# Kernel optimization log

Hardware: AMD Instinct MI355X
Metric: run time of the kernel (lower is better)

The kernel has to match this reference:

```python
import jax, jax.numpy as jnp
import numpy as np

BS, L, D, H, BLOCKS = 2, 8192, 1024, 16, 16
BC = L // BLOCKS          # block_ctx = 512
HD = D // H               # head dim = 64
SCALE2 = 1.0 / float(np.sqrt(HD))  # (scale*scale) with scale = HD**-0.25


def setup_inputs() -> dict:
    key = jax.random.key(0)
    k0, k1, k2 = jax.random.split(key, 3)
    return {
        "x": jax.random.normal(k0, (BS, L, D), jnp.float32),
        "w_attn": jax.random.normal(k1, (D, 3 * D), jnp.float32) * 0.02,
        "b_attn": jnp.zeros((3 * D,), jnp.float32),
        "w_proj": jax.random.normal(k2, (D, D), jnp.float32) * 0.02,
        "b_proj": jnp.zeros((D,), jnp.float32),
    }


def _block_attn(q, k, v):
    # q, k, v: [BS, L, D]; block-local causal attention (attn_func=1, eval path)
    nb = BS * BLOCKS
    def heads(x):
        # [BS, L, D] -> [nb, BC, D] -> [nb, H, BC, HD]
        return x.reshape(nb, BC, H, HD).transpose(0, 2, 1, 3)
    qh, kh, vh = heads(q), heads(k), heads(v)
    w = jnp.einsum('bhqd,bhkd->bhqk', qh, kh) * SCALE2          # [nb, H, BC, BC]
    w = w.astype(jnp.float32)
    mask = jnp.tril(jnp.ones((BC, BC), jnp.float32))
    w = w * mask + (-1e9) * (1.0 - mask)
    w = jax.nn.softmax(w, axis=-1)
    a = jnp.einsum('bhqk,bhkd->bhqd', w, vh)                    # [nb, H, BC, HD]
    return a.transpose(0, 2, 1, 3).reshape(BS, L, D)


def reference(x, w_attn, b_attn, w_proj, b_proj):
    qkv = x @ w_attn + b_attn                                   # Conv1D c_attn
    q, k, v = jnp.split(qkv, 3, axis=-1)
    a = _block_attn(q, k, v)
    return a @ w_proj + b_proj                                  # Conv1D c_proj
```

## Files before the change

### kernel.cpp

```cpp
#include <hip/hip_runtime.h>
#include <stdint.h>


typedef __bf16 bf16x8 __attribute__((ext_vector_type(8)));
typedef short short8 __attribute__((ext_vector_type(8)));
typedef float f32x4 __attribute__((ext_vector_type(4)));
typedef unsigned short ushort4v __attribute__((ext_vector_type(4)));
typedef unsigned short ushort8v __attribute__((ext_vector_type(8)));

#define GLOAD_LDS16(g, l)                                                      \
  __builtin_amdgcn_global_load_lds(                                            \
      (const __attribute__((address_space(1))) void*)(g),                      \
      (__attribute__((address_space(3))) void*)(l), 16, 0, 0)

static __device__ __forceinline__ f32x4 mfma16(short8 a, short8 b, f32x4 c) {
  return __builtin_amdgcn_mfma_f32_16x16x32_bf16(
      __builtin_bit_cast(bf16x8, a), __builtin_bit_cast(bf16x8, b), c, 0, 0, 0);
}

static __device__ __forceinline__ unsigned short f2bf(float f) {
  unsigned u = __builtin_bit_cast(unsigned, f);
  u += 0x7FFFu + ((u >> 16) & 1u);
  return (unsigned short)(u >> 16);
}

__global__ __launch_bounds__(256) void convert_bf16(
    const float* __restrict__ in, unsigned short* __restrict__ out, int n8) {
  for (int i = blockIdx.x * 256 + threadIdx.x; i < n8; i += gridDim.x * 256) {
    f32x4 lo = *(const f32x4*)(in + (size_t)i * 8);
    f32x4 hi = *(const f32x4*)(in + (size_t)i * 8 + 4);
    ushort8v v;
    v[0] = f2bf(lo[0]); v[1] = f2bf(lo[1]); v[2] = f2bf(lo[2]); v[3] = f2bf(lo[3]);
    v[4] = f2bf(hi[0]); v[5] = f2bf(hi[1]); v[6] = f2bf(hi[2]); v[7] = f2bf(hi[3]);
    *(ushort8v*)(out + (size_t)i * 8) = v;
  }
}

__global__ __launch_bounds__(256) void transposeW(
    const float* __restrict__ in, unsigned short* __restrict__ out,
    int K, int N) {
  __shared__ float tile[64][68];
  int tn = blockIdx.x * 64, tk = blockIdx.y * 64;
  int tid = threadIdx.x;
#pragma unroll
  for (int i = 0; i < 4; ++i) {
    int ch = i * 256 + tid;
    int r = ch >> 4, c4 = (ch & 15) << 2;
    f32x4 v = *(const f32x4*)(in + (size_t)(tk + r) * N + tn + c4);
    tile[r][c4] = v[0]; tile[r][c4 + 1] = v[1];
    tile[r][c4 + 2] = v[2]; tile[r][c4 + 3] = v[3];
  }
  __syncthreads();
#pragma unroll
  for (int i = 0; i < 4; ++i) {
    int ch = i * 256 + tid;
    int r = ch >> 4, c4 = (ch & 15) << 2;
    ushort4v v;
    v[0] = f2bf(tile[c4][r]);     v[1] = f2bf(tile[c4 + 1][r]);
    v[2] = f2bf(tile[c4 + 2][r]); v[3] = f2bf(tile[c4 + 3][r]);
    *(ushort4v*)(out + (size_t)(tn + r) * K + tk + c4) = v;
  }
}

template <bool C_F32>
__global__ __launch_bounds__(512, 2) void gemm256(
    const unsigned short* __restrict__ A, int lda,
    const unsigned short* __restrict__ Bt, int ldb,
    const float* __restrict__ bias,
    void* __restrict__ Cptr, int ldc,
    int Ntiles, int K) {
  __shared__ unsigned short sA[2][256 * 64];
  __shared__ unsigned short sB[2][256 * 64];
  int bid = blockIdx.x;
  int nwg = gridDim.x;
  int swz = (bid & 7) * (nwg >> 3) + (bid >> 3);
  int bm = swz / Ntiles, bn = swz % Ntiles;
  int tid = threadIdx.x;
  int lane = tid & 63, wave = tid >> 6;
  int wr = wave >> 2, wc = wave & 3;
  int g = lane >> 4, cx = lane & 15;

  const unsigned short* srcA[4];
  const unsigned short* srcB[4];
  int dstoff[4];
#pragma unroll
  for (int i = 0; i < 4; ++i) {
    int c = i * 512 + tid;
    int r = c >> 3, pc = c & 7;
    int cc = pc ^ (r & 7);
    srcA[i] = A + (size_t)(bm * 256 + r) * lda + cc * 8;
    srcB[i] = Bt + (size_t)(bn * 256 + r) * ldb + cc * 8;
    dstoff[i] = (i * 512 + wave * 64) * 8;
  }

  f32x4 zero4 = {0.f, 0.f, 0.f, 0.f};
  f32x4 acc[8][4];
#pragma unroll
  for (int a = 0; a < 8; ++a)
#pragma unroll
    for (int b = 0; b < 4; ++b) acc[a][b] = zero4;

  int NT = K >> 6;

  GLOAD_LDS16(srcB[0], sB[0] + dstoff[0]);
  GLOAD_LDS16(srcB[1], sB[0] + dstoff[1]);
  GLOAD_LDS16(srcB[2], sB[0] + dstoff[2]);
  GLOAD_LDS16(srcB[3], sB[0] + dstoff[3]);
  GLOAD_LDS16(srcA[0], sA[0] + dstoff[0]);
  GLOAD_LDS16(srcA[2], sA[0] + dstoff[2]);
  GLOAD_LDS16(srcA[1], sA[0] + dstoff[1]);
  GLOAD_LDS16(srcA[3], sA[0] + dstoff[3]);
  asm volatile("s_waitcnt vmcnt(2)" ::: "memory");
  __builtin_amdgcn_sched_barrier(0);
  __builtin_amdgcn_s_barrier();
  __builtin_amdgcn_sched_barrier(0);

  for (int t = 0; t < NT; ++t) {
    int p = t & 1;
    const char* bA = (const char*)sA[p];
    const char* bB = (const char*)sB[p];
    unsigned short* nA = sA[p ^ 1];
    unsigned short* nB = sB[p ^ 1];
    bool pre = (t + 1 < NT);
    int kt = (t + 1) * 64;
    short8 bfr[4][2];

#define READ_A(afv, q)                                                         \
  _Pragma("unroll") for (int mm = 0; mm < 2; ++mm)                             \
      _Pragma("unroll") for (int ks = 0; ks < 2; ++ks) {                       \
    int row = wr * 128 + ((q) * 2 + mm) * 16 + cx;                             \
    unsigned off = (unsigned)(row * 128 + ks * 64 + g * 16) ^                  \
                   ((unsigned)(row & 7) << 4);                                 \
    afv[mm][ks] = *(const short8*)(bA + off);                                  \
  }
#define MFMA_Q(afv, q)                                                         \
  __builtin_amdgcn_s_setprio(1);                                               \
  _Pragma("unroll") for (int mm = 0; mm < 2; ++mm)                             \
      _Pragma("unroll") for (int ni = 0; ni < 4; ++ni)                         \
          _Pragma("unroll") for (int ks = 0; ks < 2; ++ks)                     \
      acc[(q) * 2 + mm][ni] =                                                  \
          mfma16(afv[mm][ks], bfr[ni][ks], acc[(q) * 2 + mm][ni]);             \
  __builtin_amdgcn_s_setprio(0);
#define PHASE_TAIL()                                                           \
  __builtin_amdgcn_sched_barrier(0);                                           \
  __builtin_amdgcn_s_barrier();                                                \
  asm volatile("s_waitcnt lgkmcnt(0)" ::: "memory");                           \
  __builtin_amdgcn_sched_barrier(0);
#define PHASE_END()                                                            \
  __builtin_amdgcn_sched_barrier(0);                                           \
  __builtin_amdgcn_s_barrier();                                                \
  __builtin_amdgcn_sched_barrier(0);

    {
#pragma unroll
      for (int ni = 0; ni < 4; ++ni)
#pragma unroll
        for (int ks = 0; ks < 2; ++ks) {
          int row = wc * 64 + ni * 16 + cx;
          unsigned off = (unsigned)(row * 128 + ks * 64 + g * 16) ^
                         ((unsigned)(row & 7) << 4);
          bfr[ni][ks] = *(const short8*)(bB + off);
        }
      short8 af[2][2];
      READ_A(af, 0);
      if (pre) {
        GLOAD_LDS16(srcB[0] + kt, nB + dstoff[0]);
        GLOAD_LDS16(srcB[1] + kt, nB + dstoff[1]);
      }
      asm volatile("s_waitcnt lgkmcnt(8)" ::: "memory");
      PHASE_TAIL();
      MFMA_Q(af, 0);
      PHASE_END();
    }
    {
      short8 af[2][2];
      READ_A(af, 1);
      if (pre) {
        GLOAD_LDS16(srcB[2] + kt, nB + dstoff[2]);
        GLOAD_LDS16(srcB[3] + kt, nB + dstoff[3]);
      }
      PHASE_TAIL();
      MFMA_Q(af, 1);
      __builtin_amdgcn_sched_barrier(0);
      if (pre)
        asm volatile("s_waitcnt vmcnt(4)" ::: "memory");
      else
        asm volatile("s_waitcnt vmcnt(0)" ::: "memory");
      PHASE_END();
    }
    {
      short8 af[2][2];
      READ_A(af, 2);
      if (pre) {
        GLOAD_LDS16(srcA[0] + kt, nA + dstoff[0]);
        GLOAD_LDS16(srcA[2] + kt, nA + dstoff[2]);
      }
      PHASE_TAIL();
      MFMA_Q(af, 2);
      PHASE_END();
    }
    {
      short8 af[2][2];
      READ_A(af, 3);
      if (pre) {
        GLOAD_LDS16(srcA[1] + kt, nA + dstoff[1]);
        GLOAD_LDS16(srcA[3] + kt, nA + dstoff[3]);
      }
      PHASE_TAIL();
      MFMA_Q(af, 3);
      __builtin_amdgcn_sched_barrier(0);
      if (pre)
        asm volatile("s_waitcnt vmcnt(2)" ::: "memory");
      PHASE_END();
    }
#undef READ_A
#undef MFMA_Q
#undef PHASE_TAIL
#undef PHASE_END
  }

  float bv[4];
#pragma unroll
  for (int ni = 0; ni < 4; ++ni)
    bv[ni] = bias[bn * 256 + wc * 64 + ni * 16 + cx];

#pragma unroll
  for (int mi = 0; mi < 8; ++mi)
#pragma unroll
    for (int ni = 0; ni < 4; ++ni) {
      int col = bn * 256 + wc * 64 + ni * 16 + cx;
#pragma unroll
      for (int ri = 0; ri < 4; ++ri) {
        int row = bm * 256 + wr * 128 + mi * 16 + g * 4 + ri;
        float v = acc[mi][ni][ri] + bv[ni];
        if (C_F32)
          ((float*)Cptr)[(size_t)row * ldc + col] = v;
        else
          ((unsigned short*)Cptr)[(size_t)row * ldc + col] = f2bf(v);
      }
    }
}

__global__ __launch_bounds__(256) void attn_block(unsigned short* __restrict__ qkv) {
  const int LDQ = 3072;
  int bid = blockIdx.x;
  int pair = bid & 1;
  int nbh = bid >> 1;
  int nb = nbh >> 4, h = nbh & 15;
  int rowblk = nb << 9;
  int tid = threadIdx.x, lane = tid & 63, wave = tid >> 6;
  int g = lane >> 4, cx = lane & 15;

  __shared__ unsigned short sK[64 * 64];
  __shared__ unsigned short sVT[64 * 64];
  __shared__ unsigned short sP[4][32 * 64];
  unsigned short* myP = sP[wave];

  const unsigned short* srcK[2];
  const unsigned short* srcV[2];
  unsigned short* dstK[2];
  int kr_[2], d8_[2];
#pragma unroll
  for (int i = 0; i < 2; ++i) {
    int c = i * 256 + tid;
    int r = c >> 3, pc = c & 7, cc = pc ^ (r & 7);
    srcK[i] = qkv + (size_t)(rowblk + r) * LDQ + 1024 + h * 64 + cc * 8;
    srcV[i] = qkv + (size_t)(rowblk + r) * LDQ + 2048 + h * 64 + pc * 8;
    dstK[i] = sK + (i * 256 + wave * 64) * 8;
    kr_[i] = r; d8_[i] = pc;
  }

  f32x4 zero4 = {0.f, 0.f, 0.f, 0.f};
  const float CEXP = 0.125f * 1.44269504088896f;

  for (int qq = 0; qq < 2; ++qq) {
    int qs = qq ? (pair ? 2 : 3) : (pair ? 1 : 0);
    int ntiles = 2 * qs + 2;
    int qb0 = qs * 128 + wave * 16;

    short8 qreg[2][2];
#pragma unroll
    for (int ni = 0; ni < 2; ++ni) {
      int qrow = rowblk + qb0 + ni * 64 + cx;
      const unsigned short* qp = qkv + (size_t)qrow * LDQ + h * 64 + g * 8;
      qreg[ni][0] = *(const short8*)qp;
      qreg[ni][1] = *(const short8*)(qp + 32);
    }

    f32x4 ot[2][4];
#pragma unroll
    for (int a = 0; a < 2; ++a)
#pragma unroll
      for (int b = 0; b < 4; ++b) ot[a][b] = zero4;
    float m_run[2] = {-1e30f, -1e30f};
    float l_run[2] = {0.f, 0.f};

    for (int t = 0; t < ntiles; ++t) {
      size_t tadv = (size_t)(t * 64) * LDQ;
      short8 vv0 = *(const short8*)(srcV[0] + tadv);
      short8 vv1 = *(const short8*)(srcV[1] + tadv);
      GLOAD_LDS16(srcK[0] + tadv, dstK[0]);
      GLOAD_LDS16(srcK[1] + tadv, dstK[1]);
#pragma unroll
      for (int j = 0; j < 8; ++j) {
        int d0 = d8_[0] * 8 + j, d1 = d8_[1] * 8 + j;
        unsigned o0 = (unsigned)(d0 * 128 + kr_[0] * 2) ^
                      (unsigned)((((d8_[0] ^ j) & 7)) << 4);
        unsigned o1 = (unsigned)(d1 * 128 + kr_[1] * 2) ^
                      (unsigned)((((d8_[1] ^ j) & 7)) << 4);
        *(unsigned short*)((char*)sVT + o0) = (unsigned short)vv0[j];
        *(unsigned short*)((char*)sVT + o1) = (unsigned short)vv1[j];
      }
      __syncthreads();

      bool live0 = (t * 64) <= (qb0 + 15);

      f32x4 s[4][2];
#pragma unroll
      for (int a = 0; a < 4; ++a)
#pragma unroll
        for (int b = 0; b < 2; ++b) s[a][b] = zero4;
#pragma unroll
      for (int ks = 0; ks < 2; ++ks) {
        short8 kf[4];
#pragma unroll
        for (int mi = 0; mi < 4; ++mi) {
          int row = mi * 16 + cx;
          unsigned off = (unsigned)(row * 128 + ks * 64 + g * 16);
          off ^= (unsigned)((row & 7) << 4);
          kf[mi] = *(const short8*)((const char*)sK + off);
        }
        if (live0) {
#pragma unroll
          for (int mi = 0; mi < 4; ++mi)
            s[mi][0] = mfma16(kf[mi], qreg[0][ks], s[mi][0]);
        }
#pragma unroll
        for (int mi = 0; mi < 4; ++mi)
          s[mi][1] = mfma16(kf[mi], qreg[1][ks], s[mi][1]);
      }

      float rescv[2] = {1.f, 1.f};
#pragma unroll
      for (int ni = 0; ni < 2; ++ni) {
        if (ni == 0 && !live0) continue;
        int qbase = qb0 + ni * 64;
        int qloc = qbase + cx;
        if ((t * 64 + 63) > qbase) {
#pragma unroll
          for (int mi = 0; mi < 4; ++mi)
#pragma unroll
            for (int ri = 0; ri < 4; ++ri) {
              int kk = t * 64 + mi * 16 + g * 4 + ri;
              if (kk > qloc) s[mi][ni][ri] = -3e38f;
            }
        }
        float tm = -3e38f;
#pragma unroll
        for (int mi = 0; mi < 4; ++mi)
          tm = fmaxf(tm, fmaxf(fmaxf(s[mi][ni][0], s[mi][ni][1]),
                               fmaxf(s[mi][ni][2], s[mi][ni][3])));
        tm = fmaxf(tm, __shfl_xor(tm, 16));
        tm = fmaxf(tm, __shfl_xor(tm, 32));
        float mnew = fmaxf(m_run[ni], tm);
        float resc = exp2f((m_run[ni] - mnew) * CEXP);
        float tsum = 0.f;
#pragma unroll
        for (int mi = 0; mi < 4; ++mi)
#pragma unroll
          for (int ri = 0; ri < 4; ++ri) {
            float p = exp2f((s[mi][ni][ri] - mnew) * CEXP);
            s[mi][ni][ri] = p;
            tsum += p;
          }
        tsum += __shfl_xor(tsum, 16);
        tsum += __shfl_xor(tsum, 32);
        l_run[ni] = l_run[ni] * resc + tsum;
        m_run[ni] = mnew;
        rescv[ni] = resc;
      }

#pragma unroll
      for (int ni = 0; ni < 2; ++ni) {
        if (ni == 0 && !live0) continue;
#pragma unroll
        for (int nd = 0; nd < 4; ++nd) {
          ot[ni][nd][0] *= rescv[ni]; ot[ni][nd][1] *= rescv[ni];
          ot[ni][nd][2] *= rescv[ni]; ot[ni][nd][3] *= rescv[ni];
        }
#pragma unroll
        for (int mi = 0; mi < 4; ++mi) {
          ushort4v pk;
          pk[0] = f2bf(s[mi][ni][0]); pk[1] = f2bf(s[mi][ni][1]);
          pk[2] = f2bf(s[mi][ni][2]); pk[3] = f2bf(s[mi][ni][3]);
          int row = ni * 16 + cx;
          unsigned off = (unsigned)(row * 128 + mi * 32 + g * 8);
          off ^= (unsigned)((row & 7) << 4);
          *(ushort4v*)((char*)myP + off) = pk;
        }
      }

#pragma unroll
      for (int ks = 0; ks < 2; ++ks) {
        short8 vf[4];
#pragma unroll
        for (int nd = 0; nd < 4; ++nd) {
          int d = nd * 16 + cx;
          unsigned off = (unsigned)(d * 128 + ks * 64 + g * 16);
          off ^= (unsigned)((((d >> 3) ^ d) & 7) << 4);
          vf[nd] = *(const short8*)((const char*)sVT + off);
        }
#pragma unroll
        for (int mq = 0; mq < 2; ++mq) {
          if (mq == 0 && !live0) continue;
          int row = mq * 16 + cx;
          unsigned off = (unsigned)(row * 128 + ks * 64 + g * 16);
          off ^= (unsigned)((row & 7) << 4);
          short8 pb = *(const short8*)((const char*)myP + off);
#pragma unroll
          for (int nd = 0; nd < 4; ++nd)
            ot[mq][nd] = mfma16(vf[nd], pb, ot[mq][nd]);
        }
      }
      __syncthreads();
    }

#pragma unroll
    for (int mq = 0; mq < 2; ++mq) {
      float linv = 1.0f / fmaxf(l_run[mq], 1e-30f);
      int qrow = rowblk + qb0 + mq * 64 + cx;
#pragma unroll
      for (int nd = 0; nd < 4; ++nd) {
        ushort4v w4;
        w4[0] = f2bf(ot[mq][nd][0] * linv); w4[1] = f2bf(ot[mq][nd][1] * linv);
        w4[2] = f2bf(ot[mq][nd][2] * linv); w4[3] = f2bf(ot[mq][nd][3] * linv);
        int col = h * 64 + nd * 16 + g * 4;
        *(ushort4v*)(qkv + (size_t)qrow * LDQ + col) = w4;
      }
    }
  }
}

extern "C" void kernel_launch(void* const* d_in, const int* in_sizes, int n_in,
                              void* d_out, int out_size, void* d_ws, size_t ws_size,
                              hipStream_t stream) {
  const float* x      = (const float*)d_in[0];
  const float* w_attn = (const float*)d_in[1];
  const float* b_attn = (const float*)d_in[2];
  const float* w_proj = (const float*)d_in[3];
  const float* b_proj = (const float*)d_in[4];
  float* out = (float*)d_out;

  char* ws = (char*)d_ws;
  unsigned short* qkv = (unsigned short*)ws;
  unsigned short* wAT = (unsigned short*)(ws + (size_t)16384 * 3072 * 2);
  unsigned short* wPT = wAT + (size_t)3072 * 1024;
  unsigned short* xbf = (unsigned short*)d_out;

  transposeW<<<dim3(48, 16), 256, 0, stream>>>(w_attn, wAT, 1024, 3072);
  transposeW<<<dim3(16, 16), 256, 0, stream>>>(w_proj, wPT, 1024, 1024);
  convert_bf16<<<2048, 256, 0, stream>>>(x, xbf, 16384 * 1024 / 8);

  gemm256<false><<<768, 512, 0, stream>>>(
      xbf, 1024, wAT, 1024, b_attn, (void*)qkv, 3072, 12, 1024);

  attn_block<<<1024, 256, 0, stream>>>(qkv);

  gemm256<true><<<256, 512, 0, stream>>>(
      qkv, 3072, wPT, 1024, b_proj, (void*)out, 1024, 4, 1024);
}
```

Measured before the change: 255.3 us.

## Share K/V tile loads across both query slabs; simplify GEMM wait/barrier placement

The attention kernel previously processed its two query slabs in separate passes, each reloading K and V tiles from global memory and transposing V into LDS. Now both slabs' Q fragments and accumulators are held at once, so each K/V tile is loaded and staged once and used by both slabs. The tile count is set by the later slab, and the earlier slab is skipped once its causal range is covered. This cuts global traffic and barriers but doubles the accumulator and Q register footprint, which may lower occupancy. Separately, the GEMM drops its staged partial vmcnt waits for a full vmcnt(0) wait and barrier at the top of each k-iteration, which may reduce load/compute overlap.

```diff
diff --git a/kernel.cpp b/kernel.cpp
--- a/kernel.cpp
+++ b/kernel.cpp
@@ -110,13 +110,14 @@
   GLOAD_LDS16(srcA[2], sA[0] + dstoff[2]);
   GLOAD_LDS16(srcA[1], sA[0] + dstoff[1]);
   GLOAD_LDS16(srcA[3], sA[0] + dstoff[3]);
-  asm volatile("s_waitcnt vmcnt(2)" ::: "memory");
-  __builtin_amdgcn_sched_barrier(0);
-  __builtin_amdgcn_s_barrier();
-  __builtin_amdgcn_sched_barrier(0);
 
   for (int t = 0; t < NT; ++t) {
     int p = t & 1;
+    asm volatile("s_waitcnt vmcnt(0)" ::: "memory");
+    __builtin_amdgcn_sched_barrier(0);
+    __builtin_amdgcn_s_barrier();
+    __builtin_amdgcn_sched_barrier(0);
+
     const char* bA = (const char*)sA[p];
     const char* bB = (const char*)sB[p];
     unsigned short* nA = sA[p ^ 1];
@@ -181,11 +182,6 @@
       }
       PHASE_TAIL();
       MFMA_Q(af, 1);
-      __builtin_amdgcn_sched_barrier(0);
-      if (pre)
-        asm volatile("s_waitcnt vmcnt(4)" ::: "memory");
-      else
-        asm volatile("s_waitcnt vmcnt(0)" ::: "memory");
       PHASE_END();
     }
     {
@@ -208,9 +204,6 @@
       }
       PHASE_TAIL();
       MFMA_Q(af, 3);
-      __builtin_amdgcn_sched_barrier(0);
-      if (pre)
-        asm volatile("s_waitcnt vmcnt(2)" ::: "memory");
       PHASE_END();
     }
 #undef READ_A
@@ -270,50 +263,61 @@
     kr_[i] = r; d8_[i] = pc;
   }
 
+  int qa = pair ? 1 : 0;
+  int qb = pair ? 2 : 3;
+  int ntiles = 2 * qb + 2;
+
+  int qbase[4];
+  qbase[0] = qa * 128 + wave * 16;
+  qbase[1] = qbase[0] + 64;
+  qbase[2] = qb * 128 + wave * 16;
+  qbase[3] = qbase[2] + 64;
+
+  short8 qreg[4][2];
+#pragma unroll
+  for (int f = 0; f < 4; ++f) {
+    int qrow = rowblk + qbase[f] + cx;
+    const unsigned short* qp = qkv + (size_t)qrow * LDQ + h * 64 + g * 8;
+    qreg[f][0] = *(const short8*)qp;
+    qreg[f][1] = *(const short8*)(qp + 32);
+  }
+
   f32x4 zero4 = {0.f, 0.f, 0.f, 0.f};
+  f32x4 ot[4][4];
+#pragma unroll
+  for (int a = 0; a < 4; ++a)
+#pragma unroll
+    for (int b = 0; b < 4; ++b) ot[a][b] = zero4;
+  float m_run[4] = {-1e30f, -1e30f, -1e30f, -1e30f};
+  float l_run[4] = {0.f, 0.f, 0.f, 0.f};
+
   const float CEXP = 0.125f * 1.44269504088896f;
 
-  for (int qq = 0; qq < 2; ++qq) {
-    int qs = qq ? (pair ? 2 : 3) : (pair ? 1 : 0);
-    int ntiles = 2 * qs + 2;
-    int qb0 = qs * 128 + wave * 16;
-
-    short8 qreg[2][2];
-#pragma unroll
-    for (int ni = 0; ni < 2; ++ni) {
-      int qrow = rowblk + qb0 + ni * 64 + cx;
-      const unsigned short* qp = qkv + (size_t)qrow * LDQ + h * 64 + g * 8;
-      qreg[ni][0] = *(const short8*)qp;
-      qreg[ni][1] = *(const short8*)(qp + 32);
-    }
-
-    f32x4 ot[2][4];
-#pragma unroll
-    for (int a = 0; a < 2; ++a)
-#pragma unroll
-      for (int b = 0; b < 4; ++b) ot[a][b] = zero4;
-    float m_run[2] = {-1e30f, -1e30f};
-    float l_run[2] = {0.f, 0.f};
-
-    for (int t = 0; t < ntiles; ++t) {
-      size_t tadv = (size_t)(t * 64) * LDQ;
-      short8 vv0 = *(const short8*)(srcV[0] + tadv);
-      short8 vv1 = *(const short8*)(srcV[1] + tadv);
-      GLOAD_LDS16(srcK[0] + tadv, dstK[0]);
-      GLOAD_LDS16(srcK[1] + tadv, dstK[1]);
-#pragma unroll
-      for (int j = 0; j < 8; ++j) {
-        int d0 = d8_[0] * 8 + j, d1 = d8_[1] * 8 + j;
-        unsigned o0 = (unsigned)(d0 * 128 + kr_[0] * 2) ^
-                      (unsigned)((((d8_[0] ^ j) & 7)) << 4);
-        unsigned o1 = (unsigned)(d1 * 128 + kr_[1] * 2) ^
-                      (unsigned)((((d8_[1] ^ j) & 7)) << 4);
-        *(unsigned short*)((char*)sVT + o0) = (unsigned short)vv0[j];
-        *(unsigned short*)((char*)sVT + o1) = (unsigned short)vv1[j];
-      }
-      __syncthreads();
-
-      bool live0 = (t * 64) <= (qb0 + 15);
+  for (int t = 0; t < ntiles; ++t) {
+    size_t tadv = (size_t)(t * 64) * LDQ;
+    short8 vv0 = *(const short8*)(srcV[0] + tadv);
+    short8 vv1 = *(const short8*)(srcV[1] + tadv);
+    GLOAD_LDS16(srcK[0] + tadv, dstK[0]);
+    GLOAD_LDS16(srcK[1] + tadv, dstK[1]);
+#pragma unroll
+    for (int j = 0; j < 8; ++j) {
+      int d0 = d8_[0] * 8 + j, d1 = d8_[1] * 8 + j;
+      unsigned o0 = (unsigned)(d0 * 128 + kr_[0] * 2) ^
+                    (unsigned)((((d8_[0] ^ j) & 7)) << 4);
+      unsigned o1 = (unsigned)(d1 * 128 + kr_[1] * 2) ^
+                    (unsigned)((((d8_[1] ^ j) & 7)) << 4);
+      *(unsigned short*)((char*)sVT + o0) = (unsigned short)vv0[j];
+      *(unsigned short*)((char*)sVT + o1) = (unsigned short)vv1[j];
+    }
+    __syncthreads();
+
+    bool actA = t <= 2 * qa + 1;
+
+#pragma unroll
+    for (int halfq = 0; halfq < 2; ++halfq) {
+      if (halfq == 0 && !actA) continue;
+      int f0 = halfq * 2;
+      bool live0 = (t * 64) <= (qbase[f0] + 15);
 
       f32x4 s[4][2];
 #pragma unroll
@@ -333,20 +337,20 @@
         if (live0) {
 #pragma unroll
           for (int mi = 0; mi < 4; ++mi)
-            s[mi][0] = mfma16(kf[mi], qreg[0][ks], s[mi][0]);
+            s[mi][0] = mfma16(kf[mi], qreg[f0][ks], s[mi][0]);
         }
 #pragma unroll
         for (int mi = 0; mi < 4; ++mi)
-          s[mi][1] = mfma16(kf[mi], qreg[1][ks], s[mi][1]);
+          s[mi][1] = mfma16(kf[mi], qreg[f0 + 1][ks], s[mi][1]);
       }
 
       float rescv[2] = {1.f, 1.f};
 #pragma unroll
       for (int ni = 0; ni < 2; ++ni) {
         if (ni == 0 && !live0) continue;
-        int qbase = qb0 + ni * 64;
-        int qloc = qbase + cx;
-        if ((t * 64 + 63) > qbase) {
+        int fi = f0 + ni;
+        int qloc = qbase[fi] + cx;
+        if ((t * 64 + 63) > qbase[fi]) {
 #pragma unroll
           for (int mi = 0; mi < 4; ++mi)
 #pragma unroll
@@ -362,8 +366,8 @@
                                fmaxf(s[mi][ni][2], s[mi][ni][3])));
         tm = fmaxf(tm, __shfl_xor(tm, 16));
         tm = fmaxf(tm, __shfl_xor(tm, 32));
-        float mnew = fmaxf(m_run[ni], tm);
-        float resc = exp2f((m_run[ni] - mnew) * CEXP);
+        float mnew = fmaxf(m_run[fi], tm);
+        float resc = exp2f((m_run[fi] - mnew) * CEXP);
         float tsum = 0.f;
 #pragma unroll
         for (int mi = 0; mi < 4; ++mi)
@@ -375,18 +379,19 @@
           }
         tsum += __shfl_xor(tsum, 16);
         tsum += __shfl_xor(tsum, 32);
-        l_run[ni] = l_run[ni] * resc + tsum;
-        m_run[ni] = mnew;
+        l_run[fi] = l_run[fi] * resc + tsum;
+        m_run[fi] = mnew;
         rescv[ni] = resc;
       }
 
 #pragma unroll
       for (int ni = 0; ni < 2; ++ni) {
         if (ni == 0 && !live0) continue;
+        int fi = f0 + ni;
 #pragma unroll
         for (int nd = 0; nd < 4; ++nd) {
-          ot[ni][nd][0] *= rescv[ni]; ot[ni][nd][1] *= rescv[ni];
-          ot[ni][nd][2] *= rescv[ni]; ot[ni][nd][3] *= rescv[ni];
+          ot[fi][nd][0] *= rescv[ni]; ot[fi][nd][1] *= rescv[ni];
+          ot[fi][nd][2] *= rescv[ni]; ot[fi][nd][3] *= rescv[ni];
         }
 #pragma unroll
         for (int mi = 0; mi < 4; ++mi) {
@@ -413,30 +418,31 @@
 #pragma unroll
         for (int mq = 0; mq < 2; ++mq) {
           if (mq == 0 && !live0) continue;
+          int fi = f0 + mq;
           int row = mq * 16 + cx;
           unsigned off = (unsigned)(row * 128 + ks * 64 + g * 16);
           off ^= (unsigned)((row & 7) << 4);
           short8 pb = *(const short8*)((const char*)myP + off);
 #pragma unroll
           for (int nd = 0; nd < 4; ++nd)
-            ot[mq][nd] = mfma16(vf[nd], pb, ot[mq][nd]);
-        }
-      }
-      __syncthreads();
-    }
-
-#pragma unroll
-    for (int mq = 0; mq < 2; ++mq) {
-      float linv = 1.0f / fmaxf(l_run[mq], 1e-30f);
-      int qrow = rowblk + qb0 + mq * 64 + cx;
-#pragma unroll
-      for (int nd = 0; nd < 4; ++nd) {
-        ushort4v w4;
-        w4[0] = f2bf(ot[mq][nd][0] * linv); w4[1] = f2bf(ot[mq][nd][1] * linv);
-        w4[2] = f2bf(ot[mq][nd][2] * linv); w4[3] = f2bf(ot[mq][nd][3] * linv);
-        int col = h * 64 + nd * 16 + g * 4;
-        *(ushort4v*)(qkv + (size_t)qrow * LDQ + col) = w4;
-      }
+            ot[fi][nd] = mfma16(vf[nd], pb, ot[fi][nd]);
+        }
+      }
+    }
+    __syncthreads();
+  }
+
+#pragma unroll
+  for (int f = 0; f < 4; ++f) {
+    float linv = 1.0f / fmaxf(l_run[f], 1e-30f);
+    int qrow = rowblk + qbase[f] + cx;
+#pragma unroll
+    for (int nd = 0; nd < 4; ++nd) {
+      ushort4v w4;
+      w4[0] = f2bf(ot[f][nd][0] * linv); w4[1] = f2bf(ot[f][nd][1] * linv);
+      w4[2] = f2bf(ot[f][nd][2] * linv); w4[3] = f2bf(ot[f][nd][3] * linv);
+      int col = h * 64 + nd * 16 + g * 4;
+      *(ushort4v*)(qkv + (size_t)qrow * LDQ + col) = w4;
     }
   }
 }
```

Result: slower. 280.3 us (+9.8%).
